# Performance work log

Hardware: AMD Instinct MI355X
Metric: run time of the kernel (lower is better)

Reference implementation:

```python
import jax, jax.numpy as jnp
import numpy as np

B, F, V, E, T, NTOK, G, D = 8192, 64, 1000, 64, 2, 16, 4, 256
LN_EPS = 1e-5


def setup_inputs() -> dict:
    key = jax.random.key(0)
    ks = jax.random.split(key, 5)
    int_feats = jax.random.randint(ks[0], (B, F), 0, V, dtype=jnp.int64)
    missing_mask = jax.random.randint(ks[1], (B, F), 0, 2, dtype=jnp.int32)
    # deterministic seeded permutation of features split into NTOK equal groups
    perm = np.random.default_rng(1234).permutation(F)
    group_idx = jnp.asarray(perm.reshape(NTOK, G), dtype=jnp.int32)
    emb_tables = jax.random.normal(ks[2], (T, F, V, E), jnp.float32) * 0.02
    missing_emb = jax.random.normal(ks[3], (T, F, E), jnp.float32) * 0.02
    kW, kb = jax.random.split(ks[4])
    W = jax.random.normal(kW, (D, E * T), jnp.float32) * (1.0 / np.sqrt(E * T))
    b = jnp.zeros((D,), jnp.float32)
    ln_gamma = jnp.ones((D,), jnp.float32)
    ln_beta = jnp.zeros((D,), jnp.float32)
    return {"int_feats": int_feats, "missing_mask": missing_mask,
            "group_idx": group_idx, "emb_tables": emb_tables,
            "missing_emb": missing_emb, "W": W, "b": b,
            "ln_gamma": ln_gamma, "ln_beta": ln_beta}


def reference(int_feats, missing_mask, group_idx, emb_tables, missing_emb, W, b, ln_gamma, ln_beta):
    f_idx = jnp.arange(F)[None, :]  # (1, F) broadcast with (B, F) ids
    # per-table feature embedding gather: [T, B, F, E]
    feats = jax.vmap(lambda tbl: tbl[f_idx, int_feats])(emb_tables)
    # additive missing embeddings
    mask = missing_mask.astype(feats.dtype)
    feats = feats + mask[None, :, :, None] * missing_emb[:, None, :, :]
    # token-group mean pooling: [T, B, NTOK, G, E] -> [T, B, NTOK, E]
    pooled = feats[:, :, group_idx, :].mean(axis=3)
    # concat tables along feature dim (table order preserved): [B, NTOK, T*E]
    x = jnp.moveaxis(pooled, 0, 2).reshape(B, NTOK, T * E)
    # Linear -> SiLU -> LayerNorm
    h = jax.nn.silu(x @ W.T + b)
    mu = h.mean(-1, keepdims=True)
    var = ((h - mu) ** 2).mean(-1, keepdims=True)
    return (h - mu) * jax.lax.rsqrt(var + LN_EPS) * ln_gamma + ln_beta
```

## Files before the change

kernel.cpp:

```cpp
#include <hip/hip_runtime.h>
#include <math.h>

#define B_    8192
#define F_    64
#define V_    1000
#define E_    64
#define T_    2
#define NTOK_ 16
#define G_    4
#define D_    256
#define K_    128
#define LN_EPS 1e-5f

#define XSP   136
#define HSP   260

typedef __attribute__((ext_vector_type(8))) short  frag_ab;
typedef __attribute__((ext_vector_type(4))) float  frag_cd;

static __device__ __forceinline__ unsigned short f2bf(float f) {
    unsigned int u = __float_as_uint(f);
    u += 0x7FFFu + ((u >> 16) & 1u);
    return (unsigned short)(u >> 16);
}

__global__ __launch_bounds__(256) void convert_w_kernel(const float* __restrict__ W,
                                                        unsigned int* __restrict__ Wb_packed) {
    const int i = blockIdx.x * 256 + threadIdx.x;
    if (i < (D_ * K_) / 2) {
        const float2 v = *(const float2*)(W + (size_t)i * 2);
        Wb_packed[i] = (unsigned int)f2bf(v.x) | ((unsigned int)f2bf(v.y) << 16);
    }
}

__global__ __launch_bounds__(256) void fused_tokenizer_kernel(
    const int*   __restrict__ int_feats,
    const int*   __restrict__ missing_mask,
    const int*   __restrict__ group_idx,
    const float* __restrict__ emb_tables,
    const float* __restrict__ missing_emb,
    const unsigned short* __restrict__ Wb,
    const float* __restrict__ bias,
    const float* __restrict__ gamma,
    const float* __restrict__ beta,
    float*       __restrict__ out)
{
    __shared__ unsigned short xs[NTOK_][XSP];
    __shared__ float          hs[NTOK_][HSP];
    __shared__ int   sid[F_];
    __shared__ int   smask[F_];
    __shared__ int   sg[NTOK_ * G_];

    const int tid  = threadIdx.x;
    const int b    = blockIdx.x;
    const int lane = tid & 63;
    const int wave = tid >> 6;

    if (tid < F_) {
        sid[tid]   = int_feats[b * F_ + tid];
        smask[tid] = missing_mask[b * F_ + tid];
        sg[tid]    = group_idx[tid];
    }
    __syncthreads();

#pragma unroll
    for (int i = 0; i < 2; ++i) {
        const int c  = i * 256 + tid;
        const int n  = c >> 5;
        const int r4 = c & 31;
        const int t  = r4 >> 4;
        const int e  = (r4 & 15) * 4;
        float ax = 0.f, ay = 0.f, az = 0.f, aw = 0.f;
#pragma unroll
        for (int g = 0; g < G_; ++g) {
            const int f  = sg[n * G_ + g];
            const int id = sid[f];
            const float4 v = *(const float4*)(emb_tables + (((size_t)(t * F_ + f) * V_) + id) * E_ + e);
            float vx = v.x, vy = v.y, vz = v.z, vw = v.w;
            if (smask[f]) {
                const float4 mv = *(const float4*)(missing_emb + (size_t)(t * F_ + f) * E_ + e);
                vx += mv.x; vy += mv.y; vz += mv.z; vw += mv.w;
            }
            ax += vx; ay += vy; az += vz; aw += vw;
        }
        union { unsigned int u[2]; } pk;
        pk.u[0] = (unsigned int)f2bf(0.25f * ax) | ((unsigned int)f2bf(0.25f * ay) << 16);
        pk.u[1] = (unsigned int)f2bf(0.25f * az) | ((unsigned int)f2bf(0.25f * aw) << 16);
        *(uint2*)(&xs[n][r4 * 4]) = make_uint2(pk.u[0], pk.u[1]);
    }
    __syncthreads();

    {
        const int mA = lane & 15;
        const int q  = lane >> 4;

        frag_ab a[4];
#pragma unroll
        for (int s = 0; s < 4; ++s)
            a[s] = *(const frag_ab*)(&xs[mA][32 * s + 8 * q]);

#pragma unroll
        for (int t = 0; t < 4; ++t) {
            const int nb   = wave * 64 + t * 16;
            const int nrow = nb + mA;
            const unsigned short* wp = Wb + (size_t)nrow * K_ + 8 * q;

            frag_cd acc = {0.f, 0.f, 0.f, 0.f};
#pragma unroll
            for (int s = 0; s < 4; ++s) {
                const frag_ab bfr = *(const frag_ab*)(wp + 32 * s);
                acc = __builtin_amdgcn_mfma_f32_16x16x32_bf16(a[s], bfr, acc, 0, 0, 0);
            }
            const float bn = bias[nrow];
#pragma unroll
            for (int reg = 0; reg < 4; ++reg) {
                const int tok = q * 4 + reg;
                const float z = acc[reg] + bn;
                hs[tok][nrow] = z / (1.f + __expf(-z));
            }
        }
    }
    __syncthreads();

    {
#pragma unroll
        for (int qq = 0; qq < 4; ++qq) {
            const int n = wave * 4 + qq;
            const float4 v = *(const float4*)(&hs[n][lane * 4]);
            float s  = v.x + v.y + v.z + v.w;
            float ss = v.x * v.x + v.y * v.y + v.z * v.z + v.w * v.w;
#pragma unroll
            for (int off = 32; off > 0; off >>= 1) {
                s  += __shfl_down(s,  off, 64);
                ss += __shfl_down(ss, off, 64);
            }
            s  = __shfl(s,  0, 64);
            ss = __shfl(ss, 0, 64);
            const float mu   = s * (1.f / D_);
            const float var  = ss * (1.f / D_) - mu * mu;
            const float rsig = rsqrtf(var + LN_EPS);

            const float4 gm = *(const float4*)(gamma + lane * 4);
            const float4 bt = *(const float4*)(beta  + lane * 4);
            float4 o;
            o.x = (v.x - mu) * rsig * gm.x + bt.x;
            o.y = (v.y - mu) * rsig * gm.y + bt.y;
            o.z = (v.z - mu) * rsig * gm.z + bt.z;
            o.w = (v.w - mu) * rsig * gm.w + bt.w;
            *(float4*)(out + ((size_t)b * NTOK_ + n) * D_ + lane * 4) = o;
        }
    }
}

extern "C" void kernel_launch(void* const* d_in, const int* in_sizes, int n_in,
                              void* d_out, int out_size, void* d_ws, size_t ws_size,
                              hipStream_t stream) {
    const int*   int_feats    = (const int*)  d_in[0];
    const int*   missing_mask = (const int*)  d_in[1];
    const int*   group_idx    = (const int*)  d_in[2];
    const float* emb_tables   = (const float*)d_in[3];
    const float* missing_emb  = (const float*)d_in[4];
    const float* W            = (const float*)d_in[5];
    const float* bias         = (const float*)d_in[6];
    const float* gamma        = (const float*)d_in[7];
    const float* beta         = (const float*)d_in[8];
    float* out = (float*)d_out;

    unsigned short* Wb = (unsigned short*)d_ws;

    convert_w_kernel<<<(D_ * K_ / 2 + 255) / 256, 256, 0, stream>>>(W, (unsigned int*)Wb);
    fused_tokenizer_kernel<<<B_, 256, 0, stream>>>(
        int_feats, missing_mask, group_idx, emb_tables, missing_emb,
        Wb, bias, gamma, beta, out);
}
```

Measured before the change: 242.0 us.

## Keep SiLU outputs in registers and fuse LayerNorm stats via shuffles

Drops the shared-memory staging buffer for the post-SiLU activations. Each lane now keeps its MFMA results in registers, accumulates per-token sum and sum-of-squares, reduces them with xor shuffles inside the wave and across waves through a small shared array, then writes the normalized output straight from registers. This cuts shared memory use (the launch bounds now request higher occupancy) and removes the large LDS round trip. The cost is narrower output stores: each lane writes scalar floats strided by D instead of coalesced float4 rows. The gather also precomputes per-feature row offsets.

```diff
diff --git a/kernel.cpp b/kernel.cpp
--- a/kernel.cpp
+++ b/kernel.cpp
@@ -13,7 +13,6 @@
 #define LN_EPS 1e-5f
 
 #define XSP   136
-#define HSP   260
 
 typedef __attribute__((ext_vector_type(8))) short  frag_ab;
 typedef __attribute__((ext_vector_type(4))) float  frag_cd;
@@ -33,7 +32,7 @@
     }
 }
 
-__global__ __launch_bounds__(256) void fused_tokenizer_kernel(
+__global__ __launch_bounds__(256, 8) void fused_tokenizer_kernel(
     const int*   __restrict__ int_feats,
     const int*   __restrict__ missing_mask,
     const int*   __restrict__ group_idx,
@@ -46,20 +45,25 @@
     float*       __restrict__ out)
 {
     __shared__ unsigned short xs[NTOK_][XSP];
-    __shared__ float          hs[NTOK_][HSP];
-    __shared__ int   sid[F_];
-    __shared__ int   smask[F_];
-    __shared__ int   sg[NTOK_ * G_];
+    __shared__ unsigned int   soff[F_];
+    __shared__ int            smask[F_];
+    __shared__ int            sg[F_];
+    __shared__ float          part_s [4][NTOK_];
+    __shared__ float          part_ss[4][NTOK_];
 
     const int tid  = threadIdx.x;
     const int b    = blockIdx.x;
     const int lane = tid & 63;
     const int wave = tid >> 6;
+    const int mA   = lane & 15;
+    const int q    = lane >> 4;
 
     if (tid < F_) {
-        sid[tid]   = int_feats[b * F_ + tid];
-        smask[tid] = missing_mask[b * F_ + tid];
-        sg[tid]    = group_idx[tid];
+        const int f  = tid;
+        const int id = int_feats[b * F_ + f];
+        soff[f]  = (unsigned int)((f * V_ + id) * E_);
+        smask[f] = missing_mask[b * F_ + f];
+        sg[f]    = group_idx[f];
     }
     __syncthreads();
 
@@ -70,84 +74,104 @@
         const int r4 = c & 31;
         const int t  = r4 >> 4;
         const int e  = (r4 & 15) * 4;
+        const float* bt = emb_tables + (size_t)t * (F_ * V_ * E_) + e;
+        const float* mt = missing_emb + t * (F_ * E_) + e;
         float ax = 0.f, ay = 0.f, az = 0.f, aw = 0.f;
 #pragma unroll
         for (int g = 0; g < G_; ++g) {
-            const int f  = sg[n * G_ + g];
-            const int id = sid[f];
-            const float4 v = *(const float4*)(emb_tables + (((size_t)(t * F_ + f) * V_) + id) * E_ + e);
+            const int f = sg[n * G_ + g];
+            const float4 v = *(const float4*)(bt + soff[f]);
             float vx = v.x, vy = v.y, vz = v.z, vw = v.w;
             if (smask[f]) {
-                const float4 mv = *(const float4*)(missing_emb + (size_t)(t * F_ + f) * E_ + e);
+                const float4 mv = *(const float4*)(mt + f * E_);
                 vx += mv.x; vy += mv.y; vz += mv.z; vw += mv.w;
             }
             ax += vx; ay += vy; az += vz; aw += vw;
         }
-        union { unsigned int u[2]; } pk;
-        pk.u[0] = (unsigned int)f2bf(0.25f * ax) | ((unsigned int)f2bf(0.25f * ay) << 16);
-        pk.u[1] = (unsigned int)f2bf(0.25f * az) | ((unsigned int)f2bf(0.25f * aw) << 16);
-        *(uint2*)(&xs[n][r4 * 4]) = make_uint2(pk.u[0], pk.u[1]);
+        unsigned int p0 = (unsigned int)f2bf(0.25f * ax) | ((unsigned int)f2bf(0.25f * ay) << 16);
+        unsigned int p1 = (unsigned int)f2bf(0.25f * az) | ((unsigned int)f2bf(0.25f * aw) << 16);
+        *(uint2*)(&xs[n][r4 * 4]) = make_uint2(p0, p1);
     }
     __syncthreads();
 
-    {
-        const int mA = lane & 15;
-        const int q  = lane >> 4;
+    frag_ab a[4];
+#pragma unroll
+    for (int s = 0; s < 4; ++s)
+        a[s] = *(const frag_ab*)(&xs[mA][32 * s + 8 * q]);
 
-        frag_ab a[4];
-#pragma unroll
-        for (int s = 0; s < 4; ++s)
-            a[s] = *(const frag_ab*)(&xs[mA][32 * s + 8 * q]);
+    float hv[4][4];
+    float ps[4]  = {0.f, 0.f, 0.f, 0.f};
+    float pss[4] = {0.f, 0.f, 0.f, 0.f};
 
 #pragma unroll
-        for (int t = 0; t < 4; ++t) {
-            const int nb   = wave * 64 + t * 16;
-            const int nrow = nb + mA;
-            const unsigned short* wp = Wb + (size_t)nrow * K_ + 8 * q;
+    for (int t = 0; t < 4; ++t) {
+        const int nrow = wave * 64 + t * 16 + mA;
+        const unsigned short* wp = Wb + (size_t)nrow * K_ + 8 * q;
+        frag_cd acc = {0.f, 0.f, 0.f, 0.f};
+#pragma unroll
+        for (int s = 0; s < 4; ++s) {
+            const frag_ab bfr = *(const frag_ab*)(wp + 32 * s);
+            acc = __builtin_amdgcn_mfma_f32_16x16x32_bf16(a[s], bfr, acc, 0, 0, 0);
+        }
+        const float bn = bias[nrow];
+#pragma unroll
+        for (int reg = 0; reg < 4; ++reg) {
+            const float z = acc[reg] + bn;
+            const float h = z / (1.f + __expf(-z));
+            hv[t][reg] = h;
+            ps[reg]  += h;
+            pss[reg] += h * h;
+        }
+    }
 
-            frag_cd acc = {0.f, 0.f, 0.f, 0.f};
 #pragma unroll
-            for (int s = 0; s < 4; ++s) {
-                const frag_ab bfr = *(const frag_ab*)(wp + 32 * s);
-                acc = __builtin_amdgcn_mfma_f32_16x16x32_bf16(a[s], bfr, acc, 0, 0, 0);
-            }
-            const float bn = bias[nrow];
+    for (int off = 1; off < 16; off <<= 1) {
 #pragma unroll
-            for (int reg = 0; reg < 4; ++reg) {
-                const int tok = q * 4 + reg;
-                const float z = acc[reg] + bn;
-                hs[tok][nrow] = z / (1.f + __expf(-z));
-            }
+        for (int reg = 0; reg < 4; ++reg) {
+            ps[reg]  += __shfl_xor(ps[reg],  off, 64);
+            pss[reg] += __shfl_xor(pss[reg], off, 64);
         }
+    }
+    if (mA == 0) {
+        *(float4*)(&part_s [wave][q * 4]) = make_float4(ps[0],  ps[1],  ps[2],  ps[3]);
+        *(float4*)(&part_ss[wave][q * 4]) = make_float4(pss[0], pss[1], pss[2], pss[3]);
     }
     __syncthreads();
 
+    float4 S0 = *(const float4*)(&part_s [0][q * 4]);
+    float4 S1 = *(const float4*)(&part_s [1][q * 4]);
+    float4 S2 = *(const float4*)(&part_s [2][q * 4]);
+    float4 S3 = *(const float4*)(&part_s [3][q * 4]);
+    float4 T0 = *(const float4*)(&part_ss[0][q * 4]);
+    float4 T1 = *(const float4*)(&part_ss[1][q * 4]);
+    float4 T2 = *(const float4*)(&part_ss[2][q * 4]);
+    float4 T3 = *(const float4*)(&part_ss[3][q * 4]);
+
+    float mu[4], rs[4];
     {
+        const float s[4]  = {S0.x + S1.x + S2.x + S3.x, S0.y + S1.y + S2.y + S3.y,
+                             S0.z + S1.z + S2.z + S3.z, S0.w + S1.w + S2.w + S3.w};
+        const float ss[4] = {T0.x + T1.x + T2.x + T3.x, T0.y + T1.y + T2.y + T3.y,
+                             T0.z + T1.z + T2.z + T3.z, T0.w + T1.w + T2.w + T3.w};
 #pragma unroll
-        for (int qq = 0; qq < 4; ++qq) {
-            const int n = wave * 4 + qq;
-            const float4 v = *(const float4*)(&hs[n][lane * 4]);
-            float s  = v.x + v.y + v.z + v.w;
-            float ss = v.x * v.x + v.y * v.y + v.z * v.z + v.w * v.w;
+        for (int reg = 0; reg < 4; ++reg) {
+            mu[reg] = s[reg] * (1.f / D_);
+            const float var = ss[reg] * (1.f / D_) - mu[reg] * mu[reg];
+            rs[reg] = rsqrtf(var + LN_EPS);
+        }
+    }
+
+    const size_t obase = (size_t)b * (NTOK_ * D_);
 #pragma unroll
-            for (int off = 32; off > 0; off >>= 1) {
-                s  += __shfl_down(s,  off, 64);
-                ss += __shfl_down(ss, off, 64);
-            }
-            s  = __shfl(s,  0, 64);
-            ss = __shfl(ss, 0, 64);
-            const float mu   = s * (1.f / D_);
-            const float var  = ss * (1.f / D_) - mu * mu;
-            const float rsig = rsqrtf(var + LN_EPS);
-
-            const float4 gm = *(const float4*)(gamma + lane * 4);
-            const float4 bt = *(const float4*)(beta  + lane * 4);
-            float4 o;
-            o.x = (v.x - mu) * rsig * gm.x + bt.x;
-            o.y = (v.y - mu) * rsig * gm.y + bt.y;
-            o.z = (v.z - mu) * rsig * gm.z + bt.z;
-            o.w = (v.w - mu) * rsig * gm.w + bt.w;
-            *(float4*)(out + ((size_t)b * NTOK_ + n) * D_ + lane * 4) = o;
+    for (int t = 0; t < 4; ++t) {
+        const int col = wave * 64 + t * 16 + mA;
+        const float gm = gamma[col];
+        const float bb = beta[col];
+        float* op = out + obase + col;
+#pragma unroll
+        for (int reg = 0; reg < 4; ++reg) {
+            const int tok = q * 4 + reg;
+            op[(size_t)tok * D_] = (hv[t][reg] - mu[reg]) * rs[reg] * gm + bb;
         }
     }
 }
```

Result: no change. 245.3 us (+1.4%).
